# Performance work log

Measured on AMD Instinct MI355X. Metric: run time of the kernel, lower is better.

## Reference

```python
import jax, jax.numpy as jnp
import numpy as np

TOP_K = 8
NUM_EXPERTS = 32
CAPACITY = 1024


def setup_inputs() -> dict:
    key = jax.random.key(0)
    k1, k2, k3, k4 = jax.random.split(key, 4)
    B, S, H, E, F = 2, 1024, 1024, NUM_EXPERTS, 768
    return {
        "hidden_states": jax.random.normal(k1, (B, S, H), dtype=jnp.float32),
        "gate_weight": jax.random.normal(k2, (E, H), dtype=jnp.float32) * 0.02,
        "gate_up_proj": jax.random.normal(k3, (E, 2 * F, H), dtype=jnp.float32) * 0.02,
        "down_proj": jax.random.normal(k4, (E, H, F), dtype=jnp.float32) * 0.02,
    }


def reference(hidden_states, gate_weight, gate_up_proj, down_proj):
    B, S, H = hidden_states.shape
    E = gate_weight.shape[0]
    N = B * S
    x = hidden_states.reshape(N, H)

    # Router: fp32 softmax, top-k, renormalize (norm_topk_prob=True)
    logits = x @ gate_weight.T                                   # [N, E]
    probs = jax.nn.softmax(logits.astype(jnp.float32), axis=-1)
    topw, topi = jax.lax.top_k(probs, TOP_K)                     # [N, K]
    topw = topw / topw.sum(-1, keepdims=True)
    topw = topw.astype(x.dtype)

    # Flatten token-slot view (matches repeat_interleave ordering)
    flat_e = topi.reshape(-1)                                    # [N*K] int
    flat_w = topw.reshape(-1)                                    # [N*K]
    flat_x = jnp.repeat(x, TOP_K, axis=0)                        # [N*K, H]

    # Position of each slot within its expert (stable order, like stable argsort)
    oh = jax.nn.one_hot(flat_e, E, dtype=jnp.int32)              # [N*K, E]
    pos = (jnp.cumsum(oh, axis=0) * oh).sum(-1) - 1              # [N*K]

    # Dispatch into per-expert buffers [E, C, H]; grouped GEMMs; gather back
    buf = jnp.zeros((E, CAPACITY, H), x.dtype).at[flat_e, pos].set(flat_x, mode="drop")
    gu = jnp.einsum("ech,efh->ecf", buf, gate_up_proj)           # [E, C, 2F]
    gate, up = jnp.split(gu, 2, axis=-1)
    h = jax.nn.silu(gate) * up                                   # [E, C, F]
    eo = jnp.einsum("ecf,ehf->ech", h, down_proj)                # [E, C, H]
    tok_out = eo.at[flat_e, pos].get(mode="fill", fill_value=0)  # [N*K, H]

    out = (tok_out * flat_w[:, None]).reshape(N, TOP_K, H).sum(1)
    return out.reshape(B, S, H)
```

## Files before the change

kernel.cpp:

```cpp
#include <hip/hip_runtime.h>
#include <stdint.h>
#include <math.h>

#define NTOK  2048
#define HDIM  1024
#define FDIM  768
#define NEXP  32
#define TOPK  8
#define CAP   1024

typedef __attribute__((ext_vector_type(8))) short short8;
typedef __attribute__((ext_vector_type(4))) float f32x4;

__device__ __forceinline__ short f2bf(float f) {
  union { float f; uint32_t u; } c; c.f = f;
  uint32_t u = c.u;
  u += 0x7fffu + ((u >> 16) & 1u);
  return (short)(u >> 16);
}

__device__ __forceinline__ short8 pack8(float4 a, float4 b) {
  short8 r;
  r[0] = f2bf(a.x); r[1] = f2bf(a.y); r[2] = f2bf(a.z); r[3] = f2bf(a.w);
  r[4] = f2bf(b.x); r[5] = f2bf(b.y); r[6] = f2bf(b.z); r[7] = f2bf(b.w);
  return r;
}

__device__ __forceinline__ void gload16(const short* g, short* l) {
  __builtin_amdgcn_global_load_lds(
      (__attribute__((address_space(1))) uint32_t*)g,
      (__attribute__((address_space(3))) uint32_t*)l, 16, 0, 0);
}

__global__ __launch_bounds__(256) void cvt_gup_kern(
    const float* __restrict__ gup, short* __restrict__ gupb) {
  const size_t N8 = (size_t)NEXP * 2 * FDIM * HDIM / 8;
  const size_t stride = (size_t)gridDim.x * 256;
  for (size_t i = (size_t)blockIdx.x * 256 + threadIdx.x; i < N8; i += stride) {
    const float4 a = *(const float4*)(gup + i * 8);
    const float4 b = *(const float4*)(gup + i * 8 + 4);
    *(short8*)(gupb + i * 8) = pack8(a, b);
  }
}

__global__ __launch_bounds__(256) void cvt_dwn_kern(
    const float* __restrict__ dwn, short* __restrict__ dwnb) {
  const size_t N8 = (size_t)NEXP * HDIM * FDIM / 8;
  const size_t stride = (size_t)gridDim.x * 256;
  for (size_t i = (size_t)blockIdx.x * 256 + threadIdx.x; i < N8; i += stride) {
    const float4 a = *(const float4*)(dwn + i * 8);
    const float4 b = *(const float4*)(dwn + i * 8 + 4);
    *(short8*)(dwnb + i * 8) = pack8(a, b);
  }
}

__global__ __launch_bounds__(256) void router_kern(
    const float* __restrict__ x, const float* __restrict__ gw,
    int* __restrict__ cnt, int* __restrict__ slot_tok,
    float* __restrict__ slot_w, short* __restrict__ xb) {
  const int n0 = blockIdx.x * 8;
  const int t  = threadIdx.x;
  __shared__ float ls[8][32];

  const int e = t >> 3;
  const int j = t & 7;
  float acc[8];
#pragma unroll
  for (int i = 0; i < 8; ++i) acc[i] = 0.f;
  const float* gwe = gw + (size_t)e * HDIM;
  for (int i = 0; i < 128; ++i) {
    const int k = j + 8 * i;
    const float gv = gwe[k];
#pragma unroll
    for (int tok = 0; tok < 8; ++tok)
      acc[tok] += gv * x[(size_t)(n0 + tok) * HDIM + k];
  }
#pragma unroll
  for (int tok = 0; tok < 8; ++tok) {
    float v = acc[tok];
    v += __shfl_xor(v, 1); v += __shfl_xor(v, 2); v += __shfl_xor(v, 4);
    if (j == 0) ls[tok][e] = v;
  }
  __syncthreads();

  if (t < 8) {
    const int n = n0 + t;
    float lv[32];
#pragma unroll
    for (int i = 0; i < 32; ++i) lv[i] = ls[t][i];
    int   idx[TOPK];
    float val[TOPK];
    for (int kk = 0; kk < TOPK; ++kk) {
      float best = -INFINITY; int bi = 0;
      for (int i = 0; i < 32; ++i)
        if (lv[i] > best) { best = lv[i]; bi = i; }
      val[kk] = best; idx[kk] = bi; lv[bi] = -INFINITY;
    }
    const float m = val[0];
    float w[TOPK]; float wsum = 0.f;
    for (int kk = 0; kk < TOPK; ++kk) { w[kk] = __expf(val[kk] - m); wsum += w[kk]; }
    const float inv = 1.f / wsum;
    for (int kk = 0; kk < TOPK; ++kk) {
      const int ee = idx[kk];
      const int pos = atomicAdd(&cnt[ee], 1);
      if (pos < CAP) {
        slot_tok[ee * CAP + pos] = n * TOPK + kk;
        slot_w[ee * CAP + pos]   = w[kk] * inv;
      }
    }
  }

  const size_t base = (size_t)n0 * HDIM;
  for (int i = t; i < 8 * HDIM; i += 256)
    xb[base + i] = f2bf(x[base + i]);
}

__global__ __launch_bounds__(256) void gemm1_kern(
    const short* __restrict__ xb, const short* __restrict__ gupb,
    const int* __restrict__ cnt, const int* __restrict__ slot_tok,
    short* __restrict__ hbuf) {
  const int e = blockIdx.z;
  const int mcnt = min(cnt[e], CAP);
  const int r0 = blockIdx.y * 128;
  if (r0 >= mcnt) return;
  const int f0 = blockIdx.x * 64;

  __shared__ short As[2][128 * 32];
  __shared__ short Bg[2][64 * 32];
  __shared__ short Bu[2][64 * 32];

  const int t = threadIdx.x;
  const int wave = t >> 6, lane = t & 63;

  const int la0 = wave * 128 + lane;
  const int la1 = la0 + 64;
  const int arow0 = la0 >> 2, aseg0 = la0 & 3;
  const int arow1 = la1 >> 2, aseg1 = la1 & 3;
  int tok0 = 0, tok1 = 0;
  if (r0 + arow0 < mcnt) tok0 = slot_tok[e * CAP + r0 + arow0] >> 3;
  if (r0 + arow1 < mcnt) tok1 = slot_tok[e * CAP + r0 + arow1] >> 3;
  const short* aSrc0 = xb + (size_t)tok0 * HDIM + aseg0 * 8;
  const short* aSrc1 = xb + (size_t)tok1 * HDIM + aseg1 * 8;

  const int brow = t >> 2, bseg = t & 3;
  const short* gSrc = gupb + ((size_t)e * 1536 + f0 + brow) * HDIM + bseg * 8;
  const short* uSrc = gupb + ((size_t)e * 1536 + 768 + f0 + brow) * HDIM + bseg * 8;

  const int wm = (wave & 1) * 64, wf = (wave >> 1) * 32;
  const int lrow = lane & 15, lk = (lane >> 4) * 8;

  f32x4 accg[4][2], accu[4][2];
#pragma unroll
  for (int a = 0; a < 4; ++a)
#pragma unroll
    for (int b = 0; b < 2; ++b) {
      accg[a][b] = (f32x4){0.f, 0.f, 0.f, 0.f};
      accu[a][b] = (f32x4){0.f, 0.f, 0.f, 0.f};
    }

  auto STAGE = [&](int b, int kb) {
    gload16(aSrc0 + kb, &As[b][wave * 1024]);
    gload16(aSrc1 + kb, &As[b][wave * 1024 + 512]);
    gload16(gSrc + kb,  &Bg[b][wave * 512]);
    gload16(uSrc + kb,  &Bu[b][wave * 512]);
  };

  auto COMPUTE = [&](int b) {
    short8 af[4], bg[2], bu[2];
#pragma unroll
    for (int mt = 0; mt < 4; ++mt)
      af[mt] = *(const short8*)&As[b][(wm + mt * 16 + lrow) * 32 + lk];
#pragma unroll
    for (int nt = 0; nt < 2; ++nt) {
      bg[nt] = *(const short8*)&Bg[b][(wf + nt * 16 + lrow) * 32 + lk];
      bu[nt] = *(const short8*)&Bu[b][(wf + nt * 16 + lrow) * 32 + lk];
    }
#pragma unroll
    for (int mt = 0; mt < 4; ++mt)
#pragma unroll
      for (int nt = 0; nt < 2; ++nt) {
        accg[mt][nt] = __builtin_amdgcn_mfma_f32_16x16x32_bf16(af[mt], bg[nt], accg[mt][nt], 0, 0, 0);
        accu[mt][nt] = __builtin_amdgcn_mfma_f32_16x16x32_bf16(af[mt], bu[nt], accu[mt][nt], 0, 0, 0);
      }
  };

  STAGE(0, 0);
  __syncthreads();
  int cur = 0;
  for (int kb = 32; kb < HDIM; kb += 32) {
    STAGE(cur ^ 1, kb);
    COMPUTE(cur);
    __syncthreads();
    cur ^= 1;
  }
  COMPUTE(cur);

#pragma unroll
  for (int mt = 0; mt < 4; ++mt)
#pragma unroll
    for (int rr = 0; rr < 4; ++rr) {
      const int pos = r0 + wm + mt * 16 + (lane >> 4) * 4 + rr;
      if (pos < mcnt) {
#pragma unroll
        for (int nt = 0; nt < 2; ++nt) {
          const float g = accg[mt][nt][rr];
          const float u = accu[mt][nt][rr];
          const float hv = (g / (1.f + __expf(-g))) * u;
          hbuf[((size_t)e * CAP + pos) * FDIM + f0 + wf + nt * 16 + (lane & 15)] = f2bf(hv);
        }
      }
    }
}

__global__ __launch_bounds__(256) void gemm2_kern(
    const short* __restrict__ hbuf, const short* __restrict__ dwnb,
    const int* __restrict__ cnt, const int* __restrict__ slot_tok,
    const float* __restrict__ slot_w, float* __restrict__ slot_out) {
  const int e = blockIdx.z;
  const int mcnt = min(cnt[e], CAP);
  const int r0 = blockIdx.y * 128;
  if (r0 >= mcnt) return;
  const int n0 = blockIdx.x * 128;

  __shared__ short As[2][128 * 32];
  __shared__ short Bs[2][128 * 32];

  const int t = threadIdx.x;
  const int wave = t >> 6, lane = t & 63;

  const int l0 = wave * 128 + lane;
  const int l1 = l0 + 64;
  const int ar0 = l0 >> 2, as0 = l0 & 3;
  const int ar1 = l1 >> 2, as1 = l1 & 3;
  const short* aSrc0 = hbuf + ((size_t)e * CAP + r0 + ar0) * FDIM + as0 * 8;
  const short* aSrc1 = hbuf + ((size_t)e * CAP + r0 + ar1) * FDIM + as1 * 8;
  const short* bSrc0 = dwnb + ((size_t)e * HDIM + n0 + ar0) * FDIM + as0 * 8;
  const short* bSrc1 = dwnb + ((size_t)e * HDIM + n0 + ar1) * FDIM + as1 * 8;

  const int wm = (wave & 1) * 64, wn = (wave >> 1) * 64;
  const int lrow = lane & 15, lk = (lane >> 4) * 8;

  f32x4 acc[4][4];
#pragma unroll
  for (int a = 0; a < 4; ++a)
#pragma unroll
    for (int b = 0; b < 4; ++b) acc[a][b] = (f32x4){0.f, 0.f, 0.f, 0.f};

  auto STAGE = [&](int b, int kb) {
    gload16(aSrc0 + kb, &As[b][wave * 1024]);
    gload16(aSrc1 + kb, &As[b][wave * 1024 + 512]);
    gload16(bSrc0 + kb, &Bs[b][wave * 1024]);
    gload16(bSrc1 + kb, &Bs[b][wave * 1024 + 512]);
  };

  auto COMPUTE = [&](int b) {
    short8 af[4], bf[4];
#pragma unroll
    for (int i = 0; i < 4; ++i) {
      af[i] = *(const short8*)&As[b][(wm + i * 16 + lrow) * 32 + lk];
      bf[i] = *(const short8*)&Bs[b][(wn + i * 16 + lrow) * 32 + lk];
    }
#pragma unroll
    for (int mt = 0; mt < 4; ++mt)
#pragma unroll
      for (int nt = 0; nt < 4; ++nt)
        acc[mt][nt] = __builtin_amdgcn_mfma_f32_16x16x32_bf16(af[mt], bf[nt], acc[mt][nt], 0, 0, 0);
  };

  STAGE(0, 0);
  __syncthreads();
  int cur = 0;
  for (int kb = 32; kb < FDIM; kb += 32) {
    STAGE(cur ^ 1, kb);
    COMPUTE(cur);
    __syncthreads();
    cur ^= 1;
  }
  COMPUTE(cur);

#pragma unroll
  for (int mt = 0; mt < 4; ++mt)
#pragma unroll
    for (int rr = 0; rr < 4; ++rr) {
      const int pos = r0 + wm + mt * 16 + (lane >> 4) * 4 + rr;
      if (pos < mcnt) {
        const int s = slot_tok[e * CAP + pos];
        const float w = slot_w[e * CAP + pos];
#pragma unroll
        for (int nt = 0; nt < 4; ++nt)
          slot_out[(size_t)s * HDIM + n0 + wn + nt * 16 + (lane & 15)] = w * acc[mt][nt][rr];
      }
    }
}

__global__ __launch_bounds__(256) void gather_kern(
    const float* __restrict__ so, float* __restrict__ out) {
  const int n = blockIdx.x;
  const int c = threadIdx.x * 4;
  float4 a = make_float4(0.f, 0.f, 0.f, 0.f);
#pragma unroll
  for (int k = 0; k < TOPK; ++k) {
    const float4 v = *(const float4*)&so[((size_t)(n * TOPK + k)) * HDIM + c];
    a.x += v.x; a.y += v.y; a.z += v.z; a.w += v.w;
  }
  *(float4*)&out[(size_t)n * HDIM + c] = a;
}

extern "C" void kernel_launch(void* const* d_in, const int* in_sizes, int n_in,
                              void* d_out, int out_size, void* d_ws, size_t ws_size,
                              hipStream_t stream) {
  const float* x   = (const float*)d_in[0];
  const float* gw  = (const float*)d_in[1];
  const float* gup = (const float*)d_in[2];
  const float* dwn = (const float*)d_in[3];
  float* out = (float*)d_out;

  char* ws = (char*)d_ws;
  int*   cnt      = (int*)(ws + 0);
  int*   slot_tok = (int*)(ws + 1024);
  float* slot_w   = (float*)(ws + 1024 + 131072);
  short* xb       = (short*)(ws + 524288);
  short* hbuf     = (short*)(ws + 4718592);
  short* gupb     = (short*)(ws + 55050240);
  short* dwnb     = (short*)(ws + 155713536);
  float* slot_out = (float*)(ws + 206045184);

  hipMemsetAsync(cnt, 0, 1024, stream);
  router_kern<<<NTOK / 8, 256, 0, stream>>>(x, gw, cnt, slot_tok, slot_w, xb);
  cvt_gup_kern<<<2048, 256, 0, stream>>>(gup, gupb);
  cvt_dwn_kern<<<2048, 256, 0, stream>>>(dwn, dwnb);
  gemm1_kern<<<dim3(FDIM / 64, CAP / 128, NEXP), 256, 0, stream>>>(xb, gupb, cnt, slot_tok, hbuf);
  gemm2_kern<<<dim3(HDIM / 128, CAP / 128, NEXP), 256, 0, stream>>>(hbuf, dwnb, cnt, slot_tok, slot_w, slot_out);
  gather_kern<<<NTOK, 256, 0, stream>>>(slot_out, out);
}
```

Measured before the change: 624.1 us.

## Enlarge GEMM M-tiles to 256 rows and merge weight conversion kernels

Both grouped GEMM kernels now use 256-row M tiles, with each wave owning 64 rows across the full N tile. This doubles the accumulators per wave and reuses each loaded B tile across more rows, cutting weight traffic per FLOP. The two fp32-to-bf16 weight conversion kernels are merged into one launch. The cost is higher register pressure, possibly lower occupancy, and more wasted padded rows for experts whose token count is not a multiple of 256.

```diff
diff --git a/kernel.cpp b/kernel.cpp
--- a/kernel.cpp
+++ b/kernel.cpp
@@ -32,22 +32,19 @@
       (__attribute__((address_space(3))) uint32_t*)l, 16, 0, 0);
 }
 
-__global__ __launch_bounds__(256) void cvt_gup_kern(
-    const float* __restrict__ gup, short* __restrict__ gupb) {
-  const size_t N8 = (size_t)NEXP * 2 * FDIM * HDIM / 8;
+__global__ __launch_bounds__(256) void cvt_kern(
+    const float* __restrict__ gup, const float* __restrict__ dwn,
+    short* __restrict__ gupb, short* __restrict__ dwnb) {
+  const size_t NG8 = (size_t)NEXP * 2 * FDIM * HDIM / 8;
+  const size_t ND8 = (size_t)NEXP * HDIM * FDIM / 8;
+  const size_t tid = (size_t)blockIdx.x * 256 + threadIdx.x;
   const size_t stride = (size_t)gridDim.x * 256;
-  for (size_t i = (size_t)blockIdx.x * 256 + threadIdx.x; i < N8; i += stride) {
+  for (size_t i = tid; i < NG8; i += stride) {
     const float4 a = *(const float4*)(gup + i * 8);
     const float4 b = *(const float4*)(gup + i * 8 + 4);
     *(short8*)(gupb + i * 8) = pack8(a, b);
   }
-}
-
-__global__ __launch_bounds__(256) void cvt_dwn_kern(
-    const float* __restrict__ dwn, short* __restrict__ dwnb) {
-  const size_t N8 = (size_t)NEXP * HDIM * FDIM / 8;
-  const size_t stride = (size_t)gridDim.x * 256;
-  for (size_t i = (size_t)blockIdx.x * 256 + threadIdx.x; i < N8; i += stride) {
+  for (size_t i = tid; i < ND8; i += stride) {
     const float4 a = *(const float4*)(dwn + i * 8);
     const float4 b = *(const float4*)(dwn + i * 8 + 4);
     *(short8*)(dwnb + i * 8) = pack8(a, b);
@@ -121,64 +118,64 @@
     short* __restrict__ hbuf) {
   const int e = blockIdx.z;
   const int mcnt = min(cnt[e], CAP);
-  const int r0 = blockIdx.y * 128;
+  const int r0 = blockIdx.y * 256;
   if (r0 >= mcnt) return;
   const int f0 = blockIdx.x * 64;
 
-  __shared__ short As[2][128 * 32];
+  __shared__ short As[2][256 * 32];
   __shared__ short Bg[2][64 * 32];
   __shared__ short Bu[2][64 * 32];
 
   const int t = threadIdx.x;
   const int wave = t >> 6, lane = t & 63;
 
-  const int la0 = wave * 128 + lane;
-  const int la1 = la0 + 64;
-  const int arow0 = la0 >> 2, aseg0 = la0 & 3;
-  const int arow1 = la1 >> 2, aseg1 = la1 & 3;
-  int tok0 = 0, tok1 = 0;
-  if (r0 + arow0 < mcnt) tok0 = slot_tok[e * CAP + r0 + arow0] >> 3;
-  if (r0 + arow1 < mcnt) tok1 = slot_tok[e * CAP + r0 + arow1] >> 3;
-  const short* aSrc0 = xb + (size_t)tok0 * HDIM + aseg0 * 8;
-  const short* aSrc1 = xb + (size_t)tok1 * HDIM + aseg1 * 8;
+  const int aseg = lane & 3;
+  const short* aSrc[4];
+#pragma unroll
+  for (int i = 0; i < 4; ++i) {
+    const int row = i * 64 + wave * 16 + (lane >> 2);
+    int tok = 0;
+    if (r0 + row < mcnt) tok = slot_tok[e * CAP + r0 + row] >> 3;
+    aSrc[i] = xb + (size_t)tok * HDIM + aseg * 8;
+  }
 
   const int brow = t >> 2, bseg = t & 3;
   const short* gSrc = gupb + ((size_t)e * 1536 + f0 + brow) * HDIM + bseg * 8;
   const short* uSrc = gupb + ((size_t)e * 1536 + 768 + f0 + brow) * HDIM + bseg * 8;
 
-  const int wm = (wave & 1) * 64, wf = (wave >> 1) * 32;
   const int lrow = lane & 15, lk = (lane >> 4) * 8;
 
-  f32x4 accg[4][2], accu[4][2];
+  f32x4 accg[4][4], accu[4][4];
 #pragma unroll
   for (int a = 0; a < 4; ++a)
 #pragma unroll
-    for (int b = 0; b < 2; ++b) {
+    for (int b = 0; b < 4; ++b) {
       accg[a][b] = (f32x4){0.f, 0.f, 0.f, 0.f};
       accu[a][b] = (f32x4){0.f, 0.f, 0.f, 0.f};
     }
 
   auto STAGE = [&](int b, int kb) {
-    gload16(aSrc0 + kb, &As[b][wave * 1024]);
-    gload16(aSrc1 + kb, &As[b][wave * 1024 + 512]);
-    gload16(gSrc + kb,  &Bg[b][wave * 512]);
-    gload16(uSrc + kb,  &Bu[b][wave * 512]);
+#pragma unroll
+    for (int i = 0; i < 4; ++i)
+      gload16(aSrc[i] + kb, &As[b][i * 2048 + wave * 512]);
+    gload16(gSrc + kb, &Bg[b][wave * 512]);
+    gload16(uSrc + kb, &Bu[b][wave * 512]);
   };
 
   auto COMPUTE = [&](int b) {
-    short8 af[4], bg[2], bu[2];
+    short8 af[4], bg[4], bu[4];
 #pragma unroll
     for (int mt = 0; mt < 4; ++mt)
-      af[mt] = *(const short8*)&As[b][(wm + mt * 16 + lrow) * 32 + lk];
-#pragma unroll
-    for (int nt = 0; nt < 2; ++nt) {
-      bg[nt] = *(const short8*)&Bg[b][(wf + nt * 16 + lrow) * 32 + lk];
-      bu[nt] = *(const short8*)&Bu[b][(wf + nt * 16 + lrow) * 32 + lk];
+      af[mt] = *(const short8*)&As[b][(wave * 64 + mt * 16 + lrow) * 32 + lk];
+#pragma unroll
+    for (int nt = 0; nt < 4; ++nt) {
+      bg[nt] = *(const short8*)&Bg[b][(nt * 16 + lrow) * 32 + lk];
+      bu[nt] = *(const short8*)&Bu[b][(nt * 16 + lrow) * 32 + lk];
     }
 #pragma unroll
     for (int mt = 0; mt < 4; ++mt)
 #pragma unroll
-      for (int nt = 0; nt < 2; ++nt) {
+      for (int nt = 0; nt < 4; ++nt) {
         accg[mt][nt] = __builtin_amdgcn_mfma_f32_16x16x32_bf16(af[mt], bg[nt], accg[mt][nt], 0, 0, 0);
         accu[mt][nt] = __builtin_amdgcn_mfma_f32_16x16x32_bf16(af[mt], bu[nt], accu[mt][nt], 0, 0, 0);
       }
@@ -199,14 +196,14 @@
   for (int mt = 0; mt < 4; ++mt)
 #pragma unroll
     for (int rr = 0; rr < 4; ++rr) {
-      const int pos = r0 + wm + mt * 16 + (lane >> 4) * 4 + rr;
+      const int pos = r0 + wave * 64 + mt * 16 + (lane >> 4) * 4 + rr;
       if (pos < mcnt) {
 #pragma unroll
-        for (int nt = 0; nt < 2; ++nt) {
+        for (int nt = 0; nt < 4; ++nt) {
           const float g = accg[mt][nt][rr];
           const float u = accu[mt][nt][rr];
           const float hv = (g / (1.f + __expf(-g))) * u;
-          hbuf[((size_t)e * CAP + pos) * FDIM + f0 + wf + nt * 16 + (lane & 15)] = f2bf(hv);
+          hbuf[((size_t)e * CAP + pos) * FDIM + f0 + nt * 16 + (lane & 15)] = f2bf(hv);
         }
       }
     }
@@ -218,52 +215,55 @@
     const float* __restrict__ slot_w, float* __restrict__ slot_out) {
   const int e = blockIdx.z;
   const int mcnt = min(cnt[e], CAP);
-  const int r0 = blockIdx.y * 128;
+  const int r0 = blockIdx.y * 256;
   if (r0 >= mcnt) return;
   const int n0 = blockIdx.x * 128;
 
-  __shared__ short As[2][128 * 32];
+  __shared__ short As[2][256 * 32];
   __shared__ short Bs[2][128 * 32];
 
   const int t = threadIdx.x;
   const int wave = t >> 6, lane = t & 63;
 
-  const int l0 = wave * 128 + lane;
-  const int l1 = l0 + 64;
-  const int ar0 = l0 >> 2, as0 = l0 & 3;
-  const int ar1 = l1 >> 2, as1 = l1 & 3;
-  const short* aSrc0 = hbuf + ((size_t)e * CAP + r0 + ar0) * FDIM + as0 * 8;
-  const short* aSrc1 = hbuf + ((size_t)e * CAP + r0 + ar1) * FDIM + as1 * 8;
-  const short* bSrc0 = dwnb + ((size_t)e * HDIM + n0 + ar0) * FDIM + as0 * 8;
-  const short* bSrc1 = dwnb + ((size_t)e * HDIM + n0 + ar1) * FDIM + as1 * 8;
-
-  const int wm = (wave & 1) * 64, wn = (wave >> 1) * 64;
+  const int aseg = lane & 3;
+  const short* aSrc[4];
+#pragma unroll
+  for (int i = 0; i < 4; ++i) {
+    const int row = i * 64 + wave * 16 + (lane >> 2);
+    aSrc[i] = hbuf + ((size_t)e * CAP + r0 + row) * FDIM + aseg * 8;
+  }
+  const int brow0 = t >> 2, bseg = t & 3;
+  const short* bSrc0 = dwnb + ((size_t)e * HDIM + n0 + brow0) * FDIM + bseg * 8;
+  const short* bSrc1 = dwnb + ((size_t)e * HDIM + n0 + 64 + brow0) * FDIM + bseg * 8;
+
   const int lrow = lane & 15, lk = (lane >> 4) * 8;
 
-  f32x4 acc[4][4];
+  f32x4 acc[4][8];
 #pragma unroll
   for (int a = 0; a < 4; ++a)
 #pragma unroll
-    for (int b = 0; b < 4; ++b) acc[a][b] = (f32x4){0.f, 0.f, 0.f, 0.f};
+    for (int b = 0; b < 8; ++b) acc[a][b] = (f32x4){0.f, 0.f, 0.f, 0.f};
 
   auto STAGE = [&](int b, int kb) {
-    gload16(aSrc0 + kb, &As[b][wave * 1024]);
-    gload16(aSrc1 + kb, &As[b][wave * 1024 + 512]);
-    gload16(bSrc0 + kb, &Bs[b][wave * 1024]);
-    gload16(bSrc1 + kb, &Bs[b][wave * 1024 + 512]);
+#pragma unroll
+    for (int i = 0; i < 4; ++i)
+      gload16(aSrc[i] + kb, &As[b][i * 2048 + wave * 512]);
+    gload16(bSrc0 + kb, &Bs[b][wave * 512]);
+    gload16(bSrc1 + kb, &Bs[b][2048 + wave * 512]);
   };
 
   auto COMPUTE = [&](int b) {
-    short8 af[4], bf[4];
-#pragma unroll
-    for (int i = 0; i < 4; ++i) {
-      af[i] = *(const short8*)&As[b][(wm + i * 16 + lrow) * 32 + lk];
-      bf[i] = *(const short8*)&Bs[b][(wn + i * 16 + lrow) * 32 + lk];
-    }
+    short8 af[4], bf[8];
 #pragma unroll
     for (int mt = 0; mt < 4; ++mt)
-#pragma unroll
-      for (int nt = 0; nt < 4; ++nt)
+      af[mt] = *(const short8*)&As[b][(wave * 64 + mt * 16 + lrow) * 32 + lk];
+#pragma unroll
+    for (int nt = 0; nt < 8; ++nt)
+      bf[nt] = *(const short8*)&Bs[b][(nt * 16 + lrow) * 32 + lk];
+#pragma unroll
+    for (int mt = 0; mt < 4; ++mt)
+#pragma unroll
+      for (int nt = 0; nt < 8; ++nt)
         acc[mt][nt] = __builtin_amdgcn_mfma_f32_16x16x32_bf16(af[mt], bf[nt], acc[mt][nt], 0, 0, 0);
   };
 
@@ -282,13 +282,13 @@
   for (int mt = 0; mt < 4; ++mt)
 #pragma unroll
     for (int rr = 0; rr < 4; ++rr) {
-      const int pos = r0 + wm + mt * 16 + (lane >> 4) * 4 + rr;
+      const int pos = r0 + wave * 64 + mt * 16 + (lane >> 4) * 4 + rr;
       if (pos < mcnt) {
         const int s = slot_tok[e * CAP + pos];
         const float w = slot_w[e * CAP + pos];
 #pragma unroll
-        for (int nt = 0; nt < 4; ++nt)
-          slot_out[(size_t)s * HDIM + n0 + wn + nt * 16 + (lane & 15)] = w * acc[mt][nt][rr];
+        for (int nt = 0; nt < 8; ++nt)
+          slot_out[(size_t)s * HDIM + n0 + nt * 16 + (lane & 15)] = w * acc[mt][nt][rr];
       }
     }
 }
@@ -327,9 +327,8 @@
 
   hipMemsetAsync(cnt, 0, 1024, stream);
   router_kern<<<NTOK / 8, 256, 0, stream>>>(x, gw, cnt, slot_tok, slot_w, xb);
-  cvt_gup_kern<<<2048, 256, 0, stream>>>(gup, gupb);
-  cvt_dwn_kern<<<2048, 256, 0, stream>>>(dwn, dwnb);
-  gemm1_kern<<<dim3(FDIM / 64, CAP / 128, NEXP), 256, 0, stream>>>(xb, gupb, cnt, slot_tok, hbuf);
-  gemm2_kern<<<dim3(HDIM / 128, CAP / 128, NEXP), 256, 0, stream>>>(hbuf, dwnb, cnt, slot_tok, slot_w, slot_out);
+  cvt_kern<<<4096, 256, 0, stream>>>(gup, dwn, gupb, dwnb);
+  gemm1_kern<<<dim3(FDIM / 64, CAP / 256, NEXP), 256, 0, stream>>>(xb, gupb, cnt, slot_tok, hbuf);
+  gemm2_kern<<<dim3(HDIM / 128, CAP / 256, NEXP), 256, 0, stream>>>(hbuf, dwnb, cnt, slot_tok, slot_w, slot_out);
   gather_kern<<<NTOK, 256, 0, stream>>>(slot_out, out);
 }
```

After: 691.8 us. +10.8%, slower.
